# Kernel tuning notes

Hardware: AMD Instinct MI355X
Metric: run time of the kernel (lower is better)

## Reference

```python
import jax, jax.numpy as jnp
import numpy as np

EPS = 1e-08

def _householder(x, v):
    # x: [B,S,r], v: [B,S,r]; H x = x - 2 v_n (v_n . x), v_n = v/||v||
    v_norm_sq = jnp.sum(v * v, axis=-1, keepdims=True) + EPS
    v_n = v / jnp.sqrt(v_norm_sq)
    vTx = jnp.sum(x * v_n, axis=-1, keepdims=True)
    return x - 2.0 * v_n * vTx

def setup_inputs() -> dict:
    key = jax.random.key(0)
    ks = jax.random.split(key, 8)
    B, S, D, R = 4, 4096, 1024, 256
    N_IN, N_PROC, N_OUT, K = 16, 64, 16, 8
    x = jax.random.normal(ks[0], (B, S, D), dtype=jnp.float32)
    input_idx = jax.random.randint(ks[1], (B, S), 0, N_IN)
    process_indices = jax.random.randint(ks[2], (B, S, K), 0, N_PROC)
    output_idx = jax.random.randint(ks[3], (B, S), 0, N_OUT)
    # learned params (orthogonal-ish init approximated by scaled gaussian)
    input_neurons = jax.random.normal(ks[4], (N_IN, D, R), dtype=jnp.float32) / np.sqrt(D)
    pv = jax.random.normal(ks[5], (N_PROC, R), dtype=jnp.float32)
    process_neurons = pv / (jnp.linalg.norm(pv, axis=-1, keepdims=True) + EPS)
    output_neurons = jax.random.normal(ks[6], (N_OUT, R, D), dtype=jnp.float32) / np.sqrt(D)
    return {"x": x, "input_neurons": input_neurons, "process_neurons": process_neurons,
            "output_neurons": output_neurons, "input_idx": input_idx,
            "process_indices": process_indices, "output_idx": output_idx}

def reference(x, input_neurons, process_neurons, output_neurons,
              input_idx, process_indices, output_idx):
    # ---- input projection (hard selection): d_model -> rank ----
    # compute all-expert projections then gather per token (avoids [B,S,D,R] gather)
    all_in = jnp.einsum('bsd,ndr->bsnr', x, input_neurons)          # [B,S,n_in,R]
    h = jnp.take_along_axis(all_in, input_idx[..., None, None], axis=2)[:, :, 0, :]  # [B,S,R]
    # ---- process: k sequential Householder reflections ----
    selected_v = process_neurons[process_indices]                    # [B,S,k,R]
    vs = jnp.moveaxis(selected_v, 2, 0)                              # [k,B,S,R]
    def step(carry, v):
        return _householder(carry, v), None
    h, _ = jax.lax.scan(step, h, vs)
    # ---- output projection (hard selection): rank -> d_model ----
    all_out = jnp.einsum('bsr,nrd->bsnd', h, output_neurons)         # [B,S,n_out,D]
    out = jnp.take_along_axis(all_out, output_idx[..., None, None], axis=2)[:, :, 0, :]
    return out
```

## Files before the change

kernel.cpp:

```cpp
#include <hip/hip_runtime.h>
#include <hip/hip_bf16.h>

#define NT    16384
#define DM    1024
#define RK    256
#define N_IN  16
#define N_OUT 16
#define KHH   8
#define MAXTOK 1536
#define BM    64
#define TPE   (MAXTOK / BM)
#define KC    4
#define GEMM_BLKS (8 * TPE * 16)
#define TWOUT_BLKS (16 * 64)

typedef short bf16x8 __attribute__((ext_vector_type(8)));
typedef float f32x4 __attribute__((ext_vector_type(4)));
typedef unsigned short u16;
typedef u16 u16x8 __attribute__((ext_vector_type(8)));
typedef u16 u16x4 __attribute__((ext_vector_type(4)));

__device__ __forceinline__ u16 f2bf(float f) {
  __hip_bfloat16 b = __float2bfloat16(f);
  return *reinterpret_cast<u16*>(&b);
}
__device__ __forceinline__ float bf2f(u16 u) {
  return __uint_as_float((unsigned)u << 16);
}

__device__ __forceinline__ void gl_lds16(const void* g, void* lds) {
  __builtin_amdgcn_global_load_lds(
      (const __attribute__((address_space(1))) void*)g,
      (__attribute__((address_space(3))) void*)lds, 16, 0, 0);
}

__device__ __forceinline__ void transpose_tile(
    const float* __restrict__ src, u16* __restrict__ dst,
    int R, int C, int e, int tile, float (*ls)[65], int t) {
  const int tilesC = C >> 6;
  const int tr = (tile / tilesC) << 6;
  const int tc = (tile % tilesC) << 6;
  const int row = t >> 2, q = t & 3;
  const float* s = src + (size_t)e * R * C + (size_t)(tr + row) * C + tc + q * 16;
#pragma unroll
  for (int j = 0; j < 4; j++) {
    const float4 v = ((const float4*)s)[j];
    ls[row][q * 16 + j * 4 + 0] = v.x;
    ls[row][q * 16 + j * 4 + 1] = v.y;
    ls[row][q * 16 + j * 4 + 2] = v.z;
    ls[row][q * 16 + j * 4 + 3] = v.w;
  }
  __syncthreads();
  const int cc = t >> 2;
  u16x8 o0, o1;
#pragma unroll
  for (int j = 0; j < 8; j++) o0[j] = f2bf(ls[q * 16 + j][cc]);
#pragma unroll
  for (int j = 0; j < 8; j++) o1[j] = f2bf(ls[q * 16 + 8 + j][cc]);
  u16* d = dst + (size_t)e * C * R + (size_t)(tc + cc) * R + tr + q * 16;
  ((u16x8*)d)[0] = o0;
  ((u16x8*)d)[1] = o1;
}

__global__ __launch_bounds__(256) void lists_pn_winT(
    const int* __restrict__ in_idx, const int* __restrict__ out_idx,
    const float* __restrict__ pn, const float* __restrict__ Win,
    int* __restrict__ list_in, int* __restrict__ cnt_in,
    int* __restrict__ list_out, int* __restrict__ cnt_out,
    float* __restrict__ pnorm2, u16* __restrict__ WinT) {
  const int b = blockIdx.x;
  const int tid = threadIdx.x, lane = tid & 63, wid = tid >> 6;
  __shared__ float ls[64][65];
  __shared__ int wsum[4];

  if (b >= 33) {
    const int b2 = b - 33;
    transpose_tile(Win, WinT, DM, RK, b2 >> 6, b2 & 63, ls, tid);
    return;
  }
  if (b == 32) {
    const int p = tid >> 2, q = tid & 3;
    const float* row = pn + (size_t)p * RK + q * 64;
    float s = 0.f;
#pragma unroll
    for (int i = 0; i < 16; i++) {
      const float4 v = ((const float4*)row)[i];
      s += v.x * v.x + v.y * v.y + v.z * v.z + v.w * v.w;
    }
    s += __shfl_xor(s, 1);
    s += __shfl_xor(s, 2);
    if (q == 0) pnorm2[p] = s + 1e-8f;
    return;
  }

  const int e = b & 15, which = b >> 4;
  const int* __restrict__ idx = which ? out_idx : in_idx;
  int* __restrict__ list = (which ? list_out : list_in) + (size_t)e * NT;
  int* __restrict__ cnt = (which ? cnt_out : cnt_in) + e;

  const unsigned long long lt = (1ull << lane) - 1ull;
  int off = 0;
  for (int base = 0; base < NT; base += 1024) {
    const int4 iv = ((const int4*)(idx + base))[tid];
    const bool f0 = iv.x == e, f1 = iv.y == e, f2 = iv.z == e, f3 = iv.w == e;
    const unsigned long long m0 = __ballot(f0), m1 = __ballot(f1),
                             m2 = __ballot(f2), m3 = __ballot(f3);
    const int below = __popcll(m0 & lt) + __popcll(m1 & lt) +
                      __popcll(m2 & lt) + __popcll(m3 & lt);
    const int wtot = __popcll(m0) + __popcll(m1) + __popcll(m2) + __popcll(m3);
    if (lane == 0) wsum[wid] = wtot;
    __syncthreads();
    int b0 = 0, tot = 0;
#pragma unroll
    for (int w = 0; w < 4; w++) { if (w < wid) b0 += wsum[w]; tot += wsum[w]; }
    int pos = off + b0 + below;
    const int t = base + tid * 4;
    if (f0) list[pos++] = t;
    if (f1) list[pos++] = t + 1;
    if (f2) list[pos++] = t + 2;
    if (f3) list[pos++] = t + 3;
    off += tot;
    __syncthreads();
  }
  if (tid == 0) *cnt = off;
}

__global__ __launch_bounds__(256, 4) void input_gemm_woT(
    const float* __restrict__ x, const u16* __restrict__ WinT,
    const int* __restrict__ list, const int* __restrict__ cnt,
    u16* __restrict__ h4,
    const float* __restrict__ Wout, u16* __restrict__ WoT) {
  __shared__ __align__(16) char smem[24832];
  const int tid = threadIdx.x, lane = tid & 63, w = tid >> 6;
  const int bid = blockIdx.x;

  if (bid >= GEMM_BLKS) {
    const int b2 = bid - GEMM_BLKS;
    transpose_tile(Wout, WoT, RK, DM, b2 >> 6, b2 & 63,
                   (float(*)[65])smem, tid);
    return;
  }

  const int xcd = bid & 7;
  int j = bid >> 3;
  const int tile = j % TPE;
  j /= TPE;
  const int nb = j & 1;
  const int e = xcd * 2 + ((j >> 1) & 1);
  const int kc = j >> 2;
  const int nt = cnt[e];
  const int t0 = tile * BM;
  if (t0 >= nt) return;
  const int* __restrict__ lst = list + (size_t)e * NT + t0;
  const int ntok = min(BM, nt - t0);

  u16* As = (u16*)smem;
  u16* Bs = (u16*)(smem + 8192);
  int* toks = (int*)(smem + 8192 + 16384);

  if (tid < BM) toks[tid] = lst[tid < ntok ? tid : 0];
  __syncthreads();

  const int arow = tid >> 3, k8 = tid & 7;
  const float* axp0 = x + (size_t)toks[arow] * DM + kc * 256 + k8 * 8;
  const float* axp1 = x + (size_t)toks[arow + 32] * DM + kc * 256 + k8 * 8;
  const int aoff0 = arow * 128 + ((k8 ^ (arow & 7)) << 4);
  const int aoff1 = (arow + 32) * 128 + ((k8 ^ (arow & 7)) << 4);

  const int sub = lane >> 3;
  const int swz8 = ((lane & 7) ^ sub) * 8;
  const u16* Wbase = WinT + (size_t)e * RK * DM + (size_t)(nb * 128) * DM + kc * 256;

  f32x4 acc[4][2];
#pragma unroll
  for (int m = 0; m < 4; m++)
#pragma unroll
    for (int jx = 0; jx < 2; jx++) acc[m][jx] = (f32x4)0.f;

  const int l15 = lane & 15, lg = lane >> 4;

  float4 af[4][2][2];
#pragma unroll
  for (int p = 0; p < 4; ++p) {
    af[p][0][0] = ((const float4*)(axp0 + p * 64))[0];
    af[p][0][1] = ((const float4*)(axp0 + p * 64))[1];
    af[p][1][0] = ((const float4*)(axp1 + p * 64))[0];
    af[p][1][1] = ((const float4*)(axp1 + p * 64))[1];
  }

#pragma unroll
  for (int it = 0; it < 4; ++it) {
    const int k0 = it * 64;
    if (it) __syncthreads();
    u16x8 a0, a1;
    a0[0] = f2bf(af[it][0][0].x); a0[1] = f2bf(af[it][0][0].y);
    a0[2] = f2bf(af[it][0][0].z); a0[3] = f2bf(af[it][0][0].w);
    a0[4] = f2bf(af[it][0][1].x); a0[5] = f2bf(af[it][0][1].y);
    a0[6] = f2bf(af[it][0][1].z); a0[7] = f2bf(af[it][0][1].w);
    a1[0] = f2bf(af[it][1][0].x); a1[1] = f2bf(af[it][1][0].y);
    a1[2] = f2bf(af[it][1][0].z); a1[3] = f2bf(af[it][1][0].w);
    a1[4] = f2bf(af[it][1][1].x); a1[5] = f2bf(af[it][1][1].y);
    a1[6] = f2bf(af[it][1][1].z); a1[7] = f2bf(af[it][1][1].w);
#pragma unroll
    for (int i = 0; i < 4; ++i) {
      const int g = w * 4 + i;
      const int n = g * 8 + sub;
      gl_lds16(Wbase + (size_t)n * DM + k0 + swz8, Bs + g * 512);
    }
    *(u16x8*)((char*)As + aoff0) = a0;
    *(u16x8*)((char*)As + aoff1) = a1;
    __syncthreads();
#pragma unroll
    for (int kk = 0; kk < 2; ++kk) {
      const int sw = (((kk * 4 + lg) ^ (l15 & 7)) << 4);
      bf16x8 fa[4];
#pragma unroll
      for (int m = 0; m < 4; ++m)
        fa[m] = *(const bf16x8*)((const char*)As + (m * 16 + l15) * 128 + sw);
#pragma unroll
      for (int jx = 0; jx < 2; ++jx) {
        const int n = w * 32 + jx * 16 + l15;
        const bf16x8 fb = *(const bf16x8*)((const char*)Bs + n * 128 + sw);
#pragma unroll
        for (int m = 0; m < 4; ++m)
          acc[m][jx] = __builtin_amdgcn_mfma_f32_16x16x32_bf16(fa[m], fb, acc[m][jx], 0, 0, 0);
      }
    }
  }

  u16* hp4 = h4 + (size_t)kc * NT * RK;
#pragma unroll
  for (int m = 0; m < 4; ++m)
#pragma unroll
    for (int r = 0; r < 4; ++r) {
      const int slot = m * 16 + lg * 4 + r;
      if (slot < ntok) {
        u16* hp = hp4 + (size_t)toks[slot] * RK + nb * 128 + w * 32 + l15;
#pragma unroll
        for (int jx = 0; jx < 2; ++jx) hp[jx * 16] = f2bf(acc[m][jx][r]);
      }
    }
}

__global__ __launch_bounds__(256) void hh_k(
    const u16* __restrict__ h4, u16* __restrict__ hb,
    const float* __restrict__ pn, const float* __restrict__ pnorm2,
    const int* __restrict__ pidx) {
  const int lane = threadIdx.x & 63;
  const int t = blockIdx.x * 4 + (threadIdx.x >> 6);

  float4 hv;
  {
    const u16x4 p0 = ((const u16x4*)(h4 + ((size_t)0 * NT + t) * RK))[lane];
    const u16x4 p1 = ((const u16x4*)(h4 + ((size_t)1 * NT + t) * RK))[lane];
    const u16x4 p2 = ((const u16x4*)(h4 + ((size_t)2 * NT + t) * RK))[lane];
    const u16x4 p3 = ((const u16x4*)(h4 + ((size_t)3 * NT + t) * RK))[lane];
    hv.x = (bf2f(p0[0]) + bf2f(p1[0])) + (bf2f(p2[0]) + bf2f(p3[0]));
    hv.y = (bf2f(p0[1]) + bf2f(p1[1])) + (bf2f(p2[1]) + bf2f(p3[1]));
    hv.z = (bf2f(p0[2]) + bf2f(p1[2])) + (bf2f(p2[2]) + bf2f(p3[2]));
    hv.w = (bf2f(p0[3]) + bf2f(p1[3])) + (bf2f(p2[3]) + bf2f(p3[3]));
  }

#pragma unroll
  for (int k = 0; k < KHH; k++) {
    const int p = pidx[t * KHH + k];
    const float4 v = ((const float4*)(pn + (size_t)p * RK))[lane];
    float dvh = v.x * hv.x + v.y * hv.y + v.z * hv.z + v.w * hv.w;
#pragma unroll
    for (int s = 32; s; s >>= 1) dvh += __shfl_xor(dvh, s);
    const float c = 2.f * dvh / pnorm2[p];
    hv.x = fmaf(-c, v.x, hv.x);
    hv.y = fmaf(-c, v.y, hv.y);
    hv.z = fmaf(-c, v.z, hv.z);
    hv.w = fmaf(-c, v.w, hv.w);
  }
  u16x4 o;
  o[0] = f2bf(hv.x); o[1] = f2bf(hv.y); o[2] = f2bf(hv.z); o[3] = f2bf(hv.w);
  ((u16x4*)(hb + (size_t)t * RK))[lane] = o;
}

__global__ __launch_bounds__(256, 6) void output_gemm_mfma(
    const u16* __restrict__ hb, const u16* __restrict__ WoT,
    const int* __restrict__ list, const int* __restrict__ cnt,
    float* __restrict__ out) {
  const int bid = blockIdx.x;
  const int xcd = bid & 7;
  int j = bid >> 3;
  const int tile = j % TPE;
  j /= TPE;
  const int e = xcd * 2 + (j & 1);
  const int cb = j >> 1;
  const int nt = cnt[e];
  const int t0 = tile * BM;
  if (t0 >= nt) return;
  const int* __restrict__ lst = list + (size_t)e * NT + t0;
  const int ntok = min(BM, nt - t0);

  __shared__ __align__(16) u16 As[BM * 64];
  __shared__ __align__(16) u16 Bs[128 * 64];
  __shared__ int toks[BM];

  const int tid = threadIdx.x, lane = tid & 63, w = tid >> 6;
  if (tid < BM) toks[tid] = lst[tid < ntok ? tid : 0];
  __syncthreads();

  const int sub = lane >> 3;
  const int swz8 = ((lane & 7) ^ sub) * 8;
  const u16* Wbase = WoT + (size_t)e * DM * RK + (size_t)(cb * 128) * RK;
  const int ar0 = (w * 2 + 0) * 8 + sub;
  const int ar1 = (w * 2 + 1) * 8 + sub;
  const u16* asrc0 = hb + (size_t)toks[ar0] * RK + swz8;
  const u16* asrc1 = hb + (size_t)toks[ar1] * RK + swz8;

  f32x4 acc[4][2];
#pragma unroll
  for (int m = 0; m < 4; m++)
#pragma unroll
    for (int jx = 0; jx < 2; jx++) acc[m][jx] = (f32x4)0.f;

  const int l15 = lane & 15, lg = lane >> 4;

#pragma unroll
  for (int it = 0; it < RK / 64; ++it) {
    const int k0 = it * 64;
    if (it) __syncthreads();
    gl_lds16(asrc0 + k0, As + (w * 2 + 0) * 512);
    gl_lds16(asrc1 + k0, As + (w * 2 + 1) * 512);
#pragma unroll
    for (int i = 0; i < 4; ++i) {
      const int g = w * 4 + i;
      const int n = g * 8 + sub;
      gl_lds16(Wbase + (size_t)n * RK + k0 + swz8, Bs + g * 512);
    }
    __syncthreads();
#pragma unroll
    for (int kk = 0; kk < 2; ++kk) {
      const int sw = (((kk * 4 + lg) ^ (l15 & 7)) << 4);
      bf16x8 fa[4];
#pragma unroll
      for (int m = 0; m < 4; ++m)
        fa[m] = *(const bf16x8*)((const char*)As + (m * 16 + l15) * 128 + sw);
#pragma unroll
      for (int jx = 0; jx < 2; ++jx) {
        const int n = w * 32 + jx * 16 + l15;
        const bf16x8 fb = *(const bf16x8*)((const char*)Bs + n * 128 + sw);
#pragma unroll
        for (int m = 0; m < 4; ++m)
          acc[m][jx] = __builtin_amdgcn_mfma_f32_16x16x32_bf16(fa[m], fb, acc[m][jx], 0, 0, 0);
      }
    }
  }

#pragma unroll
  for (int m = 0; m < 4; ++m)
#pragma unroll
    for (int r = 0; r < 4; ++r) {
      const int slot = m * 16 + lg * 4 + r;
      if (slot < ntok) {
        float* op = out + (size_t)toks[slot] * DM + cb * 128 + w * 32 + l15;
#pragma unroll
        for (int jx = 0; jx < 2; ++jx) op[jx * 16] = acc[m][jx][r];
      }
    }
}

extern "C" void kernel_launch(void* const* d_in, const int* in_sizes, int n_in,
                              void* d_out, int out_size, void* d_ws,
                              size_t ws_size, hipStream_t stream) {
  const float* x     = (const float*)d_in[0];
  const float* Win   = (const float*)d_in[1];
  const float* pn    = (const float*)d_in[2];
  const float* Wout  = (const float*)d_in[3];
  const int* in_idx  = (const int*)d_in[4];
  const int* pidx    = (const int*)d_in[5];
  const int* out_idx = (const int*)d_in[6];
  float* out = (float*)d_out;

  char* ws = (char*)d_ws;
  u16* WinT  = (u16*)ws;                    ws += (size_t)N_IN * RK * DM * 2;
  u16* WoT   = (u16*)ws;                    ws += (size_t)N_OUT * DM * RK * 2;
  u16* hb    = (u16*)ws;                    ws += (size_t)NT * RK * 2;
  u16* h4    = (u16*)ws;                    ws += (size_t)KC * NT * RK * 2;
  int* list_in  = (int*)ws;                 ws += (size_t)N_IN * NT * 4;
  int* list_out = (int*)ws;                 ws += (size_t)N_OUT * NT * 4;
  int* cnt_in   = (int*)ws;                 ws += 64;
  int* cnt_out  = (int*)ws;                 ws += 64;
  float* pnorm2 = (float*)ws;

  hipLaunchKernelGGL(lists_pn_winT, dim3(33 + 1024), dim3(256), 0, stream,
                     in_idx, out_idx, pn, Win, list_in, cnt_in,
                     list_out, cnt_out, pnorm2, WinT);
  hipLaunchKernelGGL(input_gemm_woT, dim3(GEMM_BLKS + TWOUT_BLKS), dim3(256),
                     0, stream, x, WinT, list_in, cnt_in, h4, Wout, WoT);
  hipLaunchKernelGGL(hh_k, dim3(NT / 4), dim3(256), 0, stream,
                     h4, hb, pn, pnorm2, pidx);
  hipLaunchKernelGGL(output_gemm_mfma, dim3(GEMM_BLKS), dim3(256), 0, stream,
                     hb, WoT, list_out, cnt_out, out);
}
```

Baseline: 81.41 us.

## Pre-convert x to bf16 and stream A tiles via direct global-to-LDS loads

Adds a conversion stage to the first kernel that writes x as bf16 into a workspace buffer. The input GEMM then loads A tiles with global_load_lds instead of fp32 register loads plus in-register conversion. WinT is also re-laid out in K-chunks so B loads use a compact 256-wide stride, and the GEMM's launch-bounds occupancy target is raised. This cuts register pressure and per-block conversion work in the GEMM, but adds a full extra pass that reads x in fp32 and writes it back in bf16.

```diff
diff --git a/kernel.cpp b/kernel.cpp
--- a/kernel.cpp
+++ b/kernel.cpp
@@ -13,6 +13,7 @@
 #define KC    4
 #define GEMM_BLKS (8 * TPE * 16)
 #define TWOUT_BLKS (16 * 64)
+#define CVT_BLKS  2048
 
 typedef short bf16x8 __attribute__((ext_vector_type(8)));
 typedef float f32x4 __attribute__((ext_vector_type(4)));
@@ -62,20 +63,61 @@
   ((u16x8*)d)[1] = o1;
 }
 
-__global__ __launch_bounds__(256) void lists_pn_winT(
+__global__ __launch_bounds__(256) void lists_pn_winT_cvt(
     const int* __restrict__ in_idx, const int* __restrict__ out_idx,
     const float* __restrict__ pn, const float* __restrict__ Win,
+    const float* __restrict__ x,
     int* __restrict__ list_in, int* __restrict__ cnt_in,
     int* __restrict__ list_out, int* __restrict__ cnt_out,
-    float* __restrict__ pnorm2, u16* __restrict__ WinT) {
+    float* __restrict__ pnorm2, u16* __restrict__ WinT,
+    u16* __restrict__ xb) {
   const int b = blockIdx.x;
   const int tid = threadIdx.x, lane = tid & 63, wid = tid >> 6;
   __shared__ float ls[64][65];
   __shared__ int wsum[4];
 
+  if (b >= 33 + 1024) {
+    const int bc = b - (33 + 1024);
+#pragma unroll
+    for (int g = 0; g < 4; ++g) {
+      const size_t i = (size_t)bc * 256 + tid + (size_t)g * (CVT_BLKS * 256);
+      const float4 a = ((const float4*)x)[2 * i];
+      const float4 c = ((const float4*)x)[2 * i + 1];
+      u16x8 o;
+      o[0] = f2bf(a.x); o[1] = f2bf(a.y); o[2] = f2bf(a.z); o[3] = f2bf(a.w);
+      o[4] = f2bf(c.x); o[5] = f2bf(c.y); o[6] = f2bf(c.z); o[7] = f2bf(c.w);
+      ((u16x8*)xb)[i] = o;
+    }
+    return;
+  }
   if (b >= 33) {
     const int b2 = b - 33;
-    transpose_tile(Win, WinT, DM, RK, b2 >> 6, b2 & 63, ls, tid);
+    const int e = b2 >> 6, tile = b2 & 63;
+    const int tilesC = RK >> 6;
+    const int tr = (tile / tilesC) << 6;
+    const int tc = (tile % tilesC) << 6;
+    const int row = tid >> 2, q = tid & 3;
+    const float* s = Win + (size_t)e * DM * RK + (size_t)(tr + row) * RK + tc + q * 16;
+#pragma unroll
+    for (int j = 0; j < 4; j++) {
+      const float4 v = ((const float4*)s)[j];
+      ls[row][q * 16 + j * 4 + 0] = v.x;
+      ls[row][q * 16 + j * 4 + 1] = v.y;
+      ls[row][q * 16 + j * 4 + 2] = v.z;
+      ls[row][q * 16 + j * 4 + 3] = v.w;
+    }
+    __syncthreads();
+    const int cc = tid >> 2;
+    u16x8 o0, o1;
+#pragma unroll
+    for (int j = 0; j < 8; j++) o0[j] = f2bf(ls[q * 16 + j][cc]);
+#pragma unroll
+    for (int j = 0; j < 8; j++) o1[j] = f2bf(ls[q * 16 + 8 + j][cc]);
+    const int D = tr + q * 16;
+    const int kc = D >> 8, dk = D & 255;
+    u16* d = WinT + ((size_t)(e * KC + kc) * RK + (tc + cc)) * 256 + dk;
+    ((u16x8*)d)[0] = o0;
+    ((u16x8*)d)[1] = o1;
     return;
   }
   if (b == 32) {
@@ -125,8 +167,8 @@
   if (tid == 0) *cnt = off;
 }
 
-__global__ __launch_bounds__(256, 4) void input_gemm_woT(
-    const float* __restrict__ x, const u16* __restrict__ WinT,
+__global__ __launch_bounds__(256, 6) void input_gemm_woT(
+    const u16* __restrict__ xb, const u16* __restrict__ WinT,
     const int* __restrict__ list, const int* __restrict__ cnt,
     u16* __restrict__ h4,
     const float* __restrict__ Wout, u16* __restrict__ WoT) {
@@ -161,15 +203,13 @@
   if (tid < BM) toks[tid] = lst[tid < ntok ? tid : 0];
   __syncthreads();
 
-  const int arow = tid >> 3, k8 = tid & 7;
-  const float* axp0 = x + (size_t)toks[arow] * DM + kc * 256 + k8 * 8;
-  const float* axp1 = x + (size_t)toks[arow + 32] * DM + kc * 256 + k8 * 8;
-  const int aoff0 = arow * 128 + ((k8 ^ (arow & 7)) << 4);
-  const int aoff1 = (arow + 32) * 128 + ((k8 ^ (arow & 7)) << 4);
-
   const int sub = lane >> 3;
   const int swz8 = ((lane & 7) ^ sub) * 8;
-  const u16* Wbase = WinT + (size_t)e * RK * DM + (size_t)(nb * 128) * DM + kc * 256;
+  const u16* Wbase = WinT + ((size_t)(e * KC + kc) * RK + nb * 128) * 256;
+  const int ar0 = (w * 2 + 0) * 8 + sub;
+  const int ar1 = (w * 2 + 1) * 8 + sub;
+  const u16* asrc0 = xb + (size_t)toks[ar0] * DM + kc * 256 + swz8;
+  const u16* asrc1 = xb + (size_t)toks[ar1] * DM + kc * 256 + swz8;
 
   f32x4 acc[4][2];
 #pragma unroll
@@ -178,37 +218,19 @@
     for (int jx = 0; jx < 2; jx++) acc[m][jx] = (f32x4)0.f;
 
   const int l15 = lane & 15, lg = lane >> 4;
-
-  float4 af[4][2][2];
-#pragma unroll
-  for (int p = 0; p < 4; ++p) {
-    af[p][0][0] = ((const float4*)(axp0 + p * 64))[0];
-    af[p][0][1] = ((const float4*)(axp0 + p * 64))[1];
-    af[p][1][0] = ((const float4*)(axp1 + p * 64))[0];
-    af[p][1][1] = ((const float4*)(axp1 + p * 64))[1];
-  }
 
 #pragma unroll
   for (int it = 0; it < 4; ++it) {
     const int k0 = it * 64;
     if (it) __syncthreads();
-    u16x8 a0, a1;
-    a0[0] = f2bf(af[it][0][0].x); a0[1] = f2bf(af[it][0][0].y);
-    a0[2] = f2bf(af[it][0][0].z); a0[3] = f2bf(af[it][0][0].w);
-    a0[4] = f2bf(af[it][0][1].x); a0[5] = f2bf(af[it][0][1].y);
-    a0[6] = f2bf(af[it][0][1].z); a0[7] = f2bf(af[it][0][1].w);
-    a1[0] = f2bf(af[it][1][0].x); a1[1] = f2bf(af[it][1][0].y);
-    a1[2] = f2bf(af[it][1][0].z); a1[3] = f2bf(af[it][1][0].w);
-    a1[4] = f2bf(af[it][1][1].x); a1[5] = f2bf(af[it][1][1].y);
-    a1[6] = f2bf(af[it][1][1].z); a1[7] = f2bf(af[it][1][1].w);
+    gl_lds16(asrc0 + k0, As + (w * 2 + 0) * 512);
+    gl_lds16(asrc1 + k0, As + (w * 2 + 1) * 512);
 #pragma unroll
     for (int i = 0; i < 4; ++i) {
       const int g = w * 4 + i;
       const int n = g * 8 + sub;
-      gl_lds16(Wbase + (size_t)n * DM + k0 + swz8, Bs + g * 512);
-    }
-    *(u16x8*)((char*)As + aoff0) = a0;
-    *(u16x8*)((char*)As + aoff1) = a1;
+      gl_lds16(Wbase + (size_t)n * 256 + k0 + swz8, Bs + g * 512);
+    }
     __syncthreads();
 #pragma unroll
     for (int kk = 0; kk < 2; ++kk) {
@@ -381,17 +403,18 @@
   u16* WoT   = (u16*)ws;                    ws += (size_t)N_OUT * DM * RK * 2;
   u16* hb    = (u16*)ws;                    ws += (size_t)NT * RK * 2;
   u16* h4    = (u16*)ws;                    ws += (size_t)KC * NT * RK * 2;
+  u16* xb    = (u16*)ws;                    ws += (size_t)NT * DM * 2;
   int* list_in  = (int*)ws;                 ws += (size_t)N_IN * NT * 4;
   int* list_out = (int*)ws;                 ws += (size_t)N_OUT * NT * 4;
   int* cnt_in   = (int*)ws;                 ws += 64;
   int* cnt_out  = (int*)ws;                 ws += 64;
   float* pnorm2 = (float*)ws;
 
-  hipLaunchKernelGGL(lists_pn_winT, dim3(33 + 1024), dim3(256), 0, stream,
-                     in_idx, out_idx, pn, Win, list_in, cnt_in,
-                     list_out, cnt_out, pnorm2, WinT);
+  hipLaunchKernelGGL(lists_pn_winT_cvt, dim3(33 + 1024 + CVT_BLKS), dim3(256),
+                     0, stream, in_idx, out_idx, pn, Win, x, list_in, cnt_in,
+                     list_out, cnt_out, pnorm2, WinT, xb);
   hipLaunchKernelGGL(input_gemm_woT, dim3(GEMM_BLKS + TWOUT_BLKS), dim3(256),
-                     0, stream, x, WinT, list_in, cnt_in, h4, Wout, WoT);
+                     0, stream, xb, WinT, list_in, cnt_in, h4, Wout, WoT);
   hipLaunchKernelGGL(hh_k, dim3(NT / 4), dim3(256), 0, stream,
                      h4, hb, pn, pnorm2, pidx);
   hipLaunchKernelGGL(output_gemm_mfma, dim3(GEMM_BLKS), dim3(256), 0, stream,
```

Result: slower. 85.27 us (+4.7%).
